# Performance work log

Hardware: AMD Instinct MI355X
Metric: run time of the kernel (lower is better)

Reference implementation:

```python
import jax, jax.numpy as jnp
import numpy as np

N_NODES = 10000   # graph_size1 == graph_size2 (coarse graph nodes)
AS1 = 8           # arr_size1 (input block size)
AS2 = 8           # arr_size2 (output block size)
E = 320000        # number of coarse edges
B = 32            # batch
SIZE1 = N_NODES * AS1
SIZE2 = N_NODES * AS2


def setup_inputs() -> dict:
    key = jax.random.key(0)
    k1, k2, k3, k4 = jax.random.split(key, 4)
    x = jax.random.normal(k1, (B, SIZE1, 1), dtype=jnp.float32)
    indices = jax.random.randint(k2, (2, E), 0, N_NODES, dtype=jnp.int32)
    # torch init: uniform_(0,1) on values (the second uniform_ overwrote the first)
    values = jax.random.uniform(k3, (E, AS1, AS2), dtype=jnp.float32)  # v[e,i,j]
    inv = 1.0 / (E * AS1 * AS2)
    b = jax.random.uniform(k4, (SIZE2,), dtype=jnp.float32, minval=-inv, maxval=inv)
    return {"x": x, "values": values, "b": b, "indices": indices}


def reference(x, values, b, indices):
    # Expanded sparse entry: A[t0*AS2 + j, t1*AS1 + i] = values[e, i, j]
    # => out_block[t0, j] += sum_i values[e,i,j] * x_block[t1, i]
    rows = indices[0]  # output coarse node per edge
    cols = indices[1]  # input coarse node per edge
    xb = x.reshape(B, N_NODES, AS1)          # view input as coarse blocks
    xg = xb[:, cols, :]                      # (B, E, AS1) irregular gather
    contrib = jnp.einsum('bei,eij->bej', xg, values)  # (B, E, AS2)
    out = jax.ops.segment_sum(contrib.transpose(1, 0, 2), rows,
                              num_segments=N_NODES)   # (N_NODES, B, AS2)
    out = out.transpose(1, 0, 2).reshape(B, SIZE2, 1)
    return out + b[None, :, None]
```

## Files before the change

### kernel.cpp

```cpp
#include <hip/hip_runtime.h>
#include <stddef.h>

#define N_NODES 10000
#define NE 320000
#define NB 32
#define SIZE1 80000
#define SIZE2 80000
#define CAP 96

#define WS_CURSOR 0
#define WS_RECS   10000
#define WS_XT     1930000

typedef short short8 __attribute__((ext_vector_type(8)));
typedef float floatx4 __attribute__((ext_vector_type(4)));
union FragU { short8 v; ushort us[8]; uint4 u4; };

__device__ inline ushort f2bf(float f) {
  union { float f; unsigned u; } c; c.f = f;
  unsigned u = c.u;
  u += 0x7fffu + ((u >> 16) & 1u);
  return (ushort)(u >> 16);
}

__device__ inline unsigned pack2bf(float a, float b) {
  return (unsigned)f2bf(a) | ((unsigned)f2bf(b) << 16);
}

__global__ __launch_bounds__(256) void build_kernel(const float* __restrict__ x,
                                                    const int* __restrict__ idxs,
                                                    int* __restrict__ cursor,
                                                    unsigned long long* __restrict__ recs,
                                                    ushort* __restrict__ xt) {
  const int t = threadIdx.x;
  const int e = blockIdx.x * 256 + t;
  const int r = idxs[e];
  const int c = idxs[NE + e];
  const int pos = atomicAdd(&cursor[r], 1);
  if (pos < CAP)
    recs[(size_t)r * CAP + pos] = (unsigned long long)(unsigned)e |
                                  ((unsigned long long)(unsigned)c << 32);

  const int n = e >> 5;
  const int b = e & 31;
  const float* xp = x + (size_t)b * SIZE1 + n * 8;
  float4 v0 = *(const float4*)xp;
  float4 v1 = *(const float4*)(xp + 4);
  FragU f;
  f.us[0] = f2bf(v0.x); f.us[1] = f2bf(v0.y); f.us[2] = f2bf(v0.z); f.us[3] = f2bf(v0.w);
  f.us[4] = f2bf(v1.x); f.us[5] = f2bf(v1.y); f.us[6] = f2bf(v1.z); f.us[7] = f2bf(v1.w);
  *(uint4*)(xt + (size_t)n * 256 + b * 8) = f.u4;
}

__global__ __launch_bounds__(256) void gather_mfma_kernel(const ushort* __restrict__ xt,
                                                          const float* __restrict__ vals,
                                                          const float* __restrict__ bias,
                                                          const int* __restrict__ cursor,
                                                          const unsigned long long* __restrict__ recs,
                                                          float* __restrict__ out) {
  const int t = threadIdx.x;
  const int lane = t & 63;
  const int w = t >> 6;
  const int n = blockIdx.x * 4 + w;
  const int quad = lane >> 4;
  const int nn = lane & 15;
  const int deg = min(cursor[n], CAP);
  const size_t nbase = (size_t)n * CAP;

  const int laneBase = lane & 48;
  const int p = (nn >> 2) & 1;
  const bool selW = (nn & 2) != 0;
  const bool selH = (nn & 1) != 0;
  int sidx[8];
#pragma unroll
  for (int i = 0; i < 8; ++i) sidx[i] = laneBase | (i << 1) | p;

  floatx4 acc0 = {0.f, 0.f, 0.f, 0.f};
  floatx4 acc1 = {0.f, 0.f, 0.f, 0.f};

  for (int base = 0; base < deg; base += 64) {
    const int lim = min(64, deg - base);
    const unsigned long long rv = recs[nbase + base + min(lane, lim - 1)];
    const int elo = (int)(unsigned)rv;
    const int ehi = (int)(unsigned)(rv >> 32);
    const int nslots = (lim + 3) >> 2;

    for (int s = 0; s < nslots; s += 2) {
      const int le0 = s * 4 + quad;
      const int lec0 = min(le0, lim - 1);
      const int eid0 = __shfl(elo, lec0);
      const int px0  = __shfl(ehi, lec0);
      const bool ok0 = le0 < lim;
      const int le1 = (s + 1) * 4 + quad;
      const int lec1 = min(le1, lim - 1);
      const int eid1 = __shfl(elo, lec1);
      const int px1  = __shfl(ehi, lec1);
      const bool ok1 = le1 < lim;

      float4 f0 = *(const float4*)(vals + (size_t)eid0 * 64 + nn * 4);
      float4 f1 = *(const float4*)(vals + (size_t)eid1 * 64 + nn * 4);
      const ushort* xr0 = xt + (size_t)px0 * 256;
      const ushort* xr1 = xt + (size_t)px1 * 256;
      FragU alo0, ahi0, alo1, ahi1;
      alo0.u4 = *(const uint4*)(xr0 + nn * 8);
      ahi0.u4 = *(const uint4*)(xr0 + 128 + nn * 8);
      alo1.u4 = *(const uint4*)(xr1 + nn * 8);
      ahi1.u4 = *(const uint4*)(xr1 + 128 + nn * 8);

      unsigned u00 = pack2bf(f0.x, f0.y), u01 = pack2bf(f0.z, f0.w);
      unsigned u10 = pack2bf(f1.x, f1.y), u11 = pack2bf(f1.z, f1.w);
      if (!ok0) { u00 = 0; u01 = 0; }
      if (!ok1) { u10 = 0; u11 = 0; }

      FragU b0, b1;
#pragma unroll
      for (int i = 0; i < 8; ++i) {
        unsigned t00 = (unsigned)__shfl((int)u00, sidx[i]);
        unsigned t01 = (unsigned)__shfl((int)u01, sidx[i]);
        unsigned w0 = selW ? t01 : t00;
        b0.us[i] = selH ? (ushort)(w0 >> 16) : (ushort)(w0 & 0xffffu);
        unsigned t10 = (unsigned)__shfl((int)u10, sidx[i]);
        unsigned t11 = (unsigned)__shfl((int)u11, sidx[i]);
        unsigned w1 = selW ? t11 : t10;
        b1.us[i] = selH ? (ushort)(w1 >> 16) : (ushort)(w1 & 0xffffu);
      }

      acc0 = __builtin_amdgcn_mfma_f32_16x16x32_bf16(alo0.v, b0.v, acc0, 0, 0, 0);
      acc1 = __builtin_amdgcn_mfma_f32_16x16x32_bf16(ahi0.v, b0.v, acc1, 0, 0, 0);
      acc0 = __builtin_amdgcn_mfma_f32_16x16x32_bf16(alo1.v, b1.v, acc0, 0, 0, 0);
      acc1 = __builtin_amdgcn_mfma_f32_16x16x32_bf16(ahi1.v, b1.v, acc1, 0, 0, 0);
    }
  }

  if (nn < 8) {
    const float bz = bias[n * 8 + nn];
#pragma unroll
    for (int r = 0; r < 4; ++r) {
      out[(size_t)(quad * 4 + r) * SIZE2 + n * 8 + nn] = acc0[r] + bz;
      out[(size_t)(16 + quad * 4 + r) * SIZE2 + n * 8 + nn] = acc1[r] + bz;
    }
  }
}

extern "C" void kernel_launch(void* const* d_in, const int* in_sizes, int n_in,
                              void* d_out, int out_size, void* d_ws, size_t ws_size,
                              hipStream_t stream) {
  const float* x    = (const float*)d_in[0];
  const float* vals = (const float*)d_in[1];
  const float* bias = (const float*)d_in[2];
  const int*   idxs = (const int*)d_in[3];
  float* out = (float*)d_out;

  int* ws = (int*)d_ws;
  int* cursor = ws + WS_CURSOR;
  unsigned long long* recs = (unsigned long long*)(ws + WS_RECS);
  ushort* xt = (ushort*)(ws + WS_XT);

  hipMemsetAsync(cursor, 0, N_NODES * sizeof(int), stream);

  build_kernel<<<NE / 256, 256, 0, stream>>>(x, idxs, cursor, recs, xt);
  gather_mfma_kernel<<<N_NODES / 4, 256, 0, stream>>>(xt, vals, bias, cursor, recs, out);
}
```

Measured before the change: 174.8 us.

## Double-buffer gather loads in MFMA loop and reorder x transpose mapping

The gather loop is now software-pipelined with two register stages: the loads for the next pair of slots are issued before the current stage's shuffle and MFMA work runs, so memory latency can hide behind compute. The build kernel also changes its thread-to-(batch,node) mapping so consecutive threads read contiguous x rows, and it issues the x loads before the atomic. This raises register pressure and may lower occupancy, and the transposed writes to xt become strided.

```diff
diff --git a/kernel.cpp b/kernel.cpp
--- a/kernel.cpp
+++ b/kernel.cpp
@@ -33,24 +33,77 @@
                                                     unsigned long long* __restrict__ recs,
                                                     ushort* __restrict__ xt) {
   const int t = threadIdx.x;
-  const int e = blockIdx.x * 256 + t;
-  const int r = idxs[e];
-  const int c = idxs[NE + e];
+  const int g = blockIdx.x * 256 + t;
+  const int b = g / 10000;
+  const int n = g - b * 10000;
+  const float* xp = x + (size_t)b * SIZE1 + n * 8;
+  const float4 v0 = *(const float4*)xp;
+  const float4 v1 = *(const float4*)(xp + 4);
+
+  const int r = idxs[g];
+  const int c = idxs[NE + g];
   const int pos = atomicAdd(&cursor[r], 1);
   if (pos < CAP)
-    recs[(size_t)r * CAP + pos] = (unsigned long long)(unsigned)e |
+    recs[(size_t)r * CAP + pos] = (unsigned long long)(unsigned)g |
                                   ((unsigned long long)(unsigned)c << 32);
 
-  const int n = e >> 5;
-  const int b = e & 31;
-  const float* xp = x + (size_t)b * SIZE1 + n * 8;
-  float4 v0 = *(const float4*)xp;
-  float4 v1 = *(const float4*)(xp + 4);
   FragU f;
   f.us[0] = f2bf(v0.x); f.us[1] = f2bf(v0.y); f.us[2] = f2bf(v0.z); f.us[3] = f2bf(v0.w);
   f.us[4] = f2bf(v1.x); f.us[5] = f2bf(v1.y); f.us[6] = f2bf(v1.z); f.us[7] = f2bf(v1.w);
   *(uint4*)(xt + (size_t)n * 256 + b * 8) = f.u4;
 }
+
+struct Stage {
+  float4 f0, f1;
+  FragU alo0, ahi0, alo1, ahi1;
+  bool ok0, ok1;
+};
+
+#define STAGE_LOAD(ST, S)                                                    \
+  {                                                                          \
+    const int le0 = (S) * 4 + quad;                                          \
+    const int lec0 = min(le0, lim - 1);                                      \
+    const int eid0 = __shfl(elo, lec0);                                      \
+    const int px0  = __shfl(ehi, lec0);                                      \
+    ST.ok0 = le0 < lim;                                                      \
+    const int le1 = (S) * 4 + 4 + quad;                                      \
+    const int lec1 = min(le1, lim - 1);                                      \
+    const int eid1 = __shfl(elo, lec1);                                      \
+    const int px1  = __shfl(ehi, lec1);                                      \
+    ST.ok1 = le1 < lim;                                                      \
+    ST.f0 = *(const float4*)(vals + (size_t)eid0 * 64 + nn * 4);             \
+    ST.f1 = *(const float4*)(vals + (size_t)eid1 * 64 + nn * 4);             \
+    const ushort* xr0 = xt + (size_t)px0 * 256;                              \
+    const ushort* xr1 = xt + (size_t)px1 * 256;                              \
+    ST.alo0.u4 = *(const uint4*)(xr0 + nn * 8);                              \
+    ST.ahi0.u4 = *(const uint4*)(xr0 + 128 + nn * 8);                        \
+    ST.alo1.u4 = *(const uint4*)(xr1 + nn * 8);                              \
+    ST.ahi1.u4 = *(const uint4*)(xr1 + 128 + nn * 8);                        \
+  }
+
+#define STAGE_COMPUTE(ST)                                                    \
+  {                                                                          \
+    unsigned u00 = pack2bf(ST.f0.x, ST.f0.y), u01 = pack2bf(ST.f0.z, ST.f0.w); \
+    unsigned u10 = pack2bf(ST.f1.x, ST.f1.y), u11 = pack2bf(ST.f1.z, ST.f1.w); \
+    if (!ST.ok0) { u00 = 0; u01 = 0; }                                       \
+    if (!ST.ok1) { u10 = 0; u11 = 0; }                                       \
+    FragU b0, b1;                                                            \
+    _Pragma("unroll")                                                        \
+    for (int i = 0; i < 8; ++i) {                                            \
+      unsigned t00 = (unsigned)__shfl((int)u00, sidx[i]);                    \
+      unsigned t01 = (unsigned)__shfl((int)u01, sidx[i]);                    \
+      unsigned w0 = selW ? t01 : t00;                                        \
+      b0.us[i] = selH ? (ushort)(w0 >> 16) : (ushort)(w0 & 0xffffu);         \
+      unsigned t10 = (unsigned)__shfl((int)u10, sidx[i]);                    \
+      unsigned t11 = (unsigned)__shfl((int)u11, sidx[i]);                    \
+      unsigned w1 = selW ? t11 : t10;                                        \
+      b1.us[i] = selH ? (ushort)(w1 >> 16) : (ushort)(w1 & 0xffffu);         \
+    }                                                                        \
+    acc0 = __builtin_amdgcn_mfma_f32_16x16x32_bf16(ST.alo0.v, b0.v, acc0, 0, 0, 0); \
+    acc1 = __builtin_amdgcn_mfma_f32_16x16x32_bf16(ST.ahi0.v, b0.v, acc1, 0, 0, 0); \
+    acc0 = __builtin_amdgcn_mfma_f32_16x16x32_bf16(ST.alo1.v, b1.v, acc0, 0, 0, 0); \
+    acc1 = __builtin_amdgcn_mfma_f32_16x16x32_bf16(ST.ahi1.v, b1.v, acc1, 0, 0, 0); \
+  }
 
 __global__ __launch_bounds__(256) void gather_mfma_kernel(const ushort* __restrict__ xt,
                                                           const float* __restrict__ vals,
@@ -85,50 +138,26 @@
     const int ehi = (int)(unsigned)(rv >> 32);
     const int nslots = (lim + 3) >> 2;
 
-    for (int s = 0; s < nslots; s += 2) {
-      const int le0 = s * 4 + quad;
-      const int lec0 = min(le0, lim - 1);
-      const int eid0 = __shfl(elo, lec0);
-      const int px0  = __shfl(ehi, lec0);
-      const bool ok0 = le0 < lim;
-      const int le1 = (s + 1) * 4 + quad;
-      const int lec1 = min(le1, lim - 1);
-      const int eid1 = __shfl(elo, lec1);
-      const int px1  = __shfl(ehi, lec1);
-      const bool ok1 = le1 < lim;
-
-      float4 f0 = *(const float4*)(vals + (size_t)eid0 * 64 + nn * 4);
-      float4 f1 = *(const float4*)(vals + (size_t)eid1 * 64 + nn * 4);
-      const ushort* xr0 = xt + (size_t)px0 * 256;
-      const ushort* xr1 = xt + (size_t)px1 * 256;
-      FragU alo0, ahi0, alo1, ahi1;
-      alo0.u4 = *(const uint4*)(xr0 + nn * 8);
-      ahi0.u4 = *(const uint4*)(xr0 + 128 + nn * 8);
-      alo1.u4 = *(const uint4*)(xr1 + nn * 8);
-      ahi1.u4 = *(const uint4*)(xr1 + 128 + nn * 8);
-
-      unsigned u00 = pack2bf(f0.x, f0.y), u01 = pack2bf(f0.z, f0.w);
-      unsigned u10 = pack2bf(f1.x, f1.y), u11 = pack2bf(f1.z, f1.w);
-      if (!ok0) { u00 = 0; u01 = 0; }
-      if (!ok1) { u10 = 0; u11 = 0; }
-
-      FragU b0, b1;
-#pragma unroll
-      for (int i = 0; i < 8; ++i) {
-        unsigned t00 = (unsigned)__shfl((int)u00, sidx[i]);
-        unsigned t01 = (unsigned)__shfl((int)u01, sidx[i]);
-        unsigned w0 = selW ? t01 : t00;
-        b0.us[i] = selH ? (ushort)(w0 >> 16) : (ushort)(w0 & 0xffffu);
-        unsigned t10 = (unsigned)__shfl((int)u10, sidx[i]);
-        unsigned t11 = (unsigned)__shfl((int)u11, sidx[i]);
-        unsigned w1 = selW ? t11 : t10;
-        b1.us[i] = selH ? (ushort)(w1 >> 16) : (ushort)(w1 & 0xffffu);
+    Stage A, B;
+    STAGE_LOAD(A, 0);
+    int s = 0;
+    while (true) {
+      if (s + 2 < nslots) {
+        STAGE_LOAD(B, s + 2);
+        STAGE_COMPUTE(A);
+        s += 2;
+        if (s + 2 < nslots) {
+          STAGE_LOAD(A, s + 2);
+          STAGE_COMPUTE(B);
+          s += 2;
+        } else {
+          STAGE_COMPUTE(B);
+          break;
+        }
+      } else {
+        STAGE_COMPUTE(A);
+        break;
       }
-
-      acc0 = __builtin_amdgcn_mfma_f32_16x16x32_bf16(alo0.v, b0.v, acc0, 0, 0, 0);
-      acc1 = __builtin_amdgcn_mfma_f32_16x16x32_bf16(ahi0.v, b0.v, acc1, 0, 0, 0);
-      acc0 = __builtin_amdgcn_mfma_f32_16x16x32_bf16(alo1.v, b1.v, acc0, 0, 0, 0);
-      acc1 = __builtin_amdgcn_mfma_f32_16x16x32_bf16(ahi1.v, b1.v, acc1, 0, 0, 0);
     }
   }
 
```

Result: slower. 179.4 us (+2.7%).
